# Optimization experiments

Hardware: AMD Instinct MI355X
Metric: run time of the kernel (lower is better)

## Reference

```python
import jax, jax.numpy as jnp
import numpy as np

B, D_IN, H, A, L, HEADS, C = 1024, 512, 768, 5001, 4, 2, 2
N_DATA = 56000.0
NEG = -1e30


def _gru_step(x, h, Wih, Whh, bih, bhh):
    # torch nn.GRU gate order: r, z, n
    gi = x @ Wih + bih            # [B, 3H]
    gh = h @ Whh + bhh            # [B, 3H]
    i_r, i_z, i_n = jnp.split(gi, 3, axis=-1)
    h_r, h_z, h_n = jnp.split(gh, 3, axis=-1)
    r = jax.nn.sigmoid(i_r + h_r)
    z = jax.nn.sigmoid(i_z + h_z)
    n = jnp.tanh(i_n + r * h_n)
    return (1.0 - z) * n + z * h


def _atom_selector(cls, mask, Wih, Whh, bih, bhh, hW, hb, ae_w, key):
    # cls: [B, H]; mask: [B, A] int32 (mutable copy); dropout in eval mode (identity)
    h = jnp.zeros_like(cls)
    cur_in = cls
    ae_const = jax.lax.stop_gradient(ae_w)
    probs = []
    max_index = None
    rows = jnp.arange(B)
    for j in range(L):
        h = _gru_step(cur_in, h, Wih, Whh, bih, bhh)
        logits = h @ hW + hb                      # [B, A]
        if j == 0:
            col0 = jnp.where(mask.sum(axis=-1) == 0, 1, mask[:, 0])
            mask = mask.at[:, 0].set(col0)
        else:
            mask = jnp.where((max_index == 0)[:, None], 0, mask)
            mask = mask.at[:, 0].set(1)
        masked = jnp.where(mask > 0, logits, NEG)
        u = jax.random.uniform(jax.random.fold_in(key, j), (B, A), minval=1e-9, maxval=1.0)
        g = -jnp.log(-jnp.log(u))
        y_soft = jax.nn.softmax(masked + g, axis=-1)  # tau = 1
        ind = jnp.argmax(y_soft, axis=-1)             # [B]
        y_hard = jax.nn.one_hot(ind, A, dtype=y_soft.dtype)
        prob = y_hard + y_soft - jax.lax.stop_gradient(y_soft)  # straight-through
        mask = mask.at[rows, ind].set(0)              # scatter-zero chosen atoms
        probs.append(prob)
        max_index = ind
        cur_in = cls + prob @ ae_const                # atom embedding feedback
    return jnp.stack(probs, axis=1)                   # [B, L, A]


def reference(x, x_mask, W1, b1, W2, b2, W3, b3, gru_Wih, gru_Whh, gru_bih, gru_bhh,
              head_W, head_b, ae_w, ce_Wmu, ce_bmu, ce_Wcov, ce_bcov, alpha):
    # linear_base MLP
    h = jax.nn.relu(x @ W1 + b1)
    h = jax.nn.relu(h @ W2 + b2)
    h = h @ W3 + b3                                   # cls embedding [B, H]
    key = jax.random.key(42)
    atom_probs, cps = [], []
    for i in range(HEADS):
        ap = _atom_selector(h, x_mask, gru_Wih[i], gru_Whh[i], gru_bih[i], gru_bhh[i],
                            head_W[i], head_b[i], ae_w, jax.random.fold_in(key, i))
        atom_probs.append(ap)
        # consequent estimator stand-in: mu [B,C], coverage [B]
        pooled = ap.mean(axis=1)                      # [B, A]
        mu = jax.nn.sigmoid(pooled @ ce_Wmu + ce_bmu)
        coverage = jax.nn.sigmoid(pooled @ ce_Wcov + ce_bcov)
        n = coverage * N_DATA
        sf = (alpha[0] / n)[:, None]                  # [B, 1] -> broadcast to [B, C]
        cp = (mu + sf) / (1.0 + 2.0 * sf)
        cps.append(cp)
    mat_cp = jnp.stack(cps, axis=1)                   # [B, HEADS, C]
    out = jnp.log(mat_cp.mean(axis=1))                # [B, C]
    return out, jnp.stack(atom_probs, axis=1), mat_cp


def setup_inputs() -> dict:
    key = jax.random.key(0)
    ks = jax.random.split(key, 16)
    s = 0.02
    nrm = lambda k, sh: jax.random.normal(k, sh, dtype=jnp.float32) * s
    return {
        'x': jax.random.normal(ks[0], (B, D_IN), dtype=jnp.float32),
        'x_mask': jax.random.randint(ks[1], (B, A), 0, 2, dtype=jnp.int32),
        'W1': nrm(ks[2], (D_IN, H)), 'b1': jnp.zeros((H,), jnp.float32),
        'W2': nrm(ks[3], (H, H)), 'b2': jnp.zeros((H,), jnp.float32),
        'W3': nrm(ks[4], (H, H)), 'b3': jnp.zeros((H,), jnp.float32),
        'gru_Wih': nrm(ks[5], (HEADS, H, 3 * H)), 'gru_Whh': nrm(ks[6], (HEADS, H, 3 * H)),
        'gru_bih': jnp.zeros((HEADS, 3 * H), jnp.float32), 'gru_bhh': jnp.zeros((HEADS, 3 * H), jnp.float32),
        'head_W': nrm(ks[7], (HEADS, H, A)), 'head_b': jnp.zeros((HEADS, A), jnp.float32),
        'ae_w': nrm(ks[8], (A, H)),
        'ce_Wmu': nrm(ks[9], (A, C)), 'ce_bmu': jnp.zeros((C,), jnp.float32),
        'ce_Wcov': nrm(ks[10], (A,)), 'ce_bcov': jnp.zeros((), jnp.float32),
        'alpha': jnp.ones((1,), jnp.float32),
    }
```

## Files before the change

### kernel.cpp

```cpp
#include <hip/hip_runtime.h>
#include <hip/hip_bf16.h>
#include <stdint.h>
#include <stddef.h>

#define B_DIM   1024
#define DIN     512
#define H_DIM   768
#define A_DIM   5001
#define NHEADS  2
#define NSTEPS  4
#define C_DIM   2
#define NEG_VAL -1e30f
#define BH      (B_DIM * H_DIM)

typedef unsigned short u16;
typedef __attribute__((ext_vector_type(8))) short v8s;
typedef __attribute__((ext_vector_type(4))) float v4f;

typedef const __attribute__((address_space(1))) uint32_t* gas_ptr;
typedef __attribute__((address_space(3))) uint32_t* las_ptr;

__device__ __forceinline__ void load_lds16(const void* g, void* l) {
  __builtin_amdgcn_global_load_lds((gas_ptr)g, (las_ptr)l, 16, 0, 0);
}

__host__ __device__ inline uint32_t rotl32(uint32_t x, int d) {
  return (x << d) | (x >> (32 - d));
}

__host__ __device__ inline void threefry2x32(uint32_t k0, uint32_t k1,
                                             uint32_t x0, uint32_t x1,
                                             uint32_t& o0, uint32_t& o1) {
  uint32_t ks2 = k0 ^ k1 ^ 0x1BD11BDAu;
  x0 += k0; x1 += k1;
#define TFR(d) { x0 += x1; x1 = rotl32(x1, (d)); x1 ^= x0; }
  TFR(13) TFR(15) TFR(26) TFR(6)  x0 += k1;  x1 += ks2 + 1u;
  TFR(17) TFR(29) TFR(16) TFR(24) x0 += ks2; x1 += k0 + 2u;
  TFR(13) TFR(15) TFR(26) TFR(6)  x0 += k0;  x1 += k1 + 3u;
  TFR(17) TFR(29) TFR(16) TFR(24) x0 += k1;  x1 += ks2 + 4u;
  TFR(13) TFR(15) TFR(26) TFR(6)  x0 += ks2; x1 += k0 + 5u;
#undef TFR
  o0 = x0; o1 = x1;
}

__device__ inline float gumbel_noise(uint32_t k0, uint32_t k1, uint32_t idx) {
  uint32_t o0, o1;
  threefry2x32(k0, k1, 0u, idx, o0, o1);
  uint32_t bits = o0 ^ o1;
  float f = __uint_as_float(0x3f800000u | (bits >> 9)) - 1.0f;
  float u = fmaxf(1e-9f, f * (1.0f - 1e-9f) + 1e-9f);
  return -logf(-logf(u));
}

__device__ inline float sigmoidf_(float x) { return 0.5f * tanhf(0.5f * x) + 0.5f; }

__device__ inline void split_bf16(float x, u16& hi, u16& lo) {
  __hip_bfloat16 h = __float2bfloat16(x);
  float hf = __bfloat162float(h);
  __hip_bfloat16 l = __float2bfloat16(x - hf);
  hi = *(const u16*)&h;
  lo = *(const u16*)&l;
}

__global__ __launch_bounds__(256) void split_kernel(
    const float* __restrict__ in, u16* __restrict__ hi, u16* __restrict__ lo, int n) {
  int idx = blockIdx.x * blockDim.x + threadIdx.x;
  if (idx >= n) return;
  u16 h, l;
  split_bf16(in[idx], h, l);
  hi[idx] = h; lo[idx] = l;
}

struct TS { const float* W; u16* hi; u16* lo; int K; int N; };
struct TS9 { TS t[9]; };

__global__ __launch_bounds__(256) void transpose_split_b(TS9 ts) {
  const TS p = ts.t[blockIdx.z];
  const int k0 = blockIdx.y * 32, n0 = blockIdx.x * 32;
  if (k0 >= p.K || n0 >= p.N) return;
  __shared__ float tile[32][33];
  const int tx = threadIdx.x & 31, ty = threadIdx.x >> 5;
#pragma unroll
  for (int r = ty; r < 32; r += 8) {
    int n = n0 + tx;
    tile[r][tx] = (n < p.N) ? p.W[(size_t)(k0 + r) * p.N + n] : 0.0f;
  }
  __syncthreads();
#pragma unroll
  for (int r = ty; r < 32; r += 8) {
    int n = n0 + r, k = k0 + tx;
    if (n < p.N) {
      u16 h, l;
      split_bf16(tile[tx][r], h, l);
      p.hi[(size_t)n * p.K + k] = h;
      p.lo[(size_t)n * p.K + k] = l;
    }
  }
}

struct GemmS {
  const u16* Ah[4]; const u16* Al[4];
  const u16* Bh[4]; const u16* Bl[4];
  const float* bias[4];
  float* C[4];
  u16* Ch[4]; u16* Cl[4];
  int N[4]; int nbx[4]; long long ldc[4]; int act[4]; int dup[4];
};

__global__ __launch_bounds__(256, 2) void gemm_mfma(GemmS gs, int K, int nby) {
  const int e = blockIdx.y;
  const int nwg = gridDim.x;
  const int chunk = nwg >> 3;
  const int lid = (blockIdx.x & 7) * chunk + (blockIdx.x >> 3);
  const int by = lid % nby;
  const int bx = lid / nby;
  if (bx >= gs.nbx[e]) return;
  const int bm = by * 128, bn = bx * 128;
  const int N = gs.N[e];

  __shared__ __align__(16) u16 lds[4][128 * 64];

  const int tid = threadIdx.x;
  const int wv = tid >> 6, ln = tid & 63;
  const int wr = wv >> 1, wc = wv & 1;
  const int lk = ln >> 4;
  const int lm = ln & 15;

  const int lrow8 = ln >> 3;
  const int sslot = (ln & 7) ^ lrow8;
  const u16* tsrc = (wv == 0) ? gs.Ah[e] : (wv == 1) ? gs.Al[e]
                  : (wv == 2) ? gs.Bh[e] : gs.Bl[e];
  const int isB = (wv >= 2);
  const int rowbase = isB ? bn : bm;

  v4f acc[4][4];
#pragma unroll
  for (int i = 0; i < 4; ++i)
#pragma unroll
    for (int j = 0; j < 4; ++j) acc[i][j] = (v4f){0.f, 0.f, 0.f, 0.f};

  for (int k0 = 0; k0 < K; k0 += 64) {
#pragma unroll
    for (int i = 0; i < 16; ++i) {
      int gr = rowbase + i * 8 + lrow8;
      if (isB && gr >= N) gr = N - 1;
      const u16* gp = tsrc + (size_t)gr * K + k0 + sslot * 8;
      load_lds16(gp, (void*)&lds[wv][i * 512]);
    }
    __syncthreads();

#pragma unroll
    for (int kh = 0; kh < 2; ++kh) {
      v8s ah[4], al[4], bh[4], bl[4];
#pragma unroll
      for (int mi = 0; mi < 4; ++mi) {
        const int r = wr * 64 + mi * 16 + lm;
        const int off = r * 64 + (((kh * 4 + lk) ^ (r & 7)) * 8);
        ah[mi] = *(const v8s*)&lds[0][off];
        al[mi] = *(const v8s*)&lds[1][off];
      }
#pragma unroll
      for (int ni = 0; ni < 4; ++ni) {
        const int r = wc * 64 + ni * 16 + lm;
        const int off = r * 64 + (((kh * 4 + lk) ^ (r & 7)) * 8);
        bh[ni] = *(const v8s*)&lds[2][off];
        bl[ni] = *(const v8s*)&lds[3][off];
      }
#pragma unroll
      for (int mi = 0; mi < 4; ++mi)
#pragma unroll
        for (int ni = 0; ni < 4; ++ni)
          acc[mi][ni] = __builtin_amdgcn_mfma_f32_16x16x32_bf16(ah[mi], bh[ni], acc[mi][ni], 0, 0, 0);
#pragma unroll
      for (int mi = 0; mi < 4; ++mi)
#pragma unroll
        for (int ni = 0; ni < 4; ++ni)
          acc[mi][ni] = __builtin_amdgcn_mfma_f32_16x16x32_bf16(ah[mi], bl[ni], acc[mi][ni], 0, 0, 0);
#pragma unroll
      for (int mi = 0; mi < 4; ++mi)
#pragma unroll
        for (int ni = 0; ni < 4; ++ni)
          acc[mi][ni] = __builtin_amdgcn_mfma_f32_16x16x32_bf16(al[mi], bh[ni], acc[mi][ni], 0, 0, 0);
    }

    __syncthreads();
  }

  const float* bias = gs.bias[e];
  const long long ldc = gs.ldc[e];
  const int act = gs.act[e];
  float* Cf = gs.C[e];
  u16* ch = gs.Ch[e]; u16* cl = gs.Cl[e];
  const int dup = gs.dup[e];
#pragma unroll
  for (int mi = 0; mi < 4; ++mi) {
    const int m = bm + wr * 64 + mi * 16 + lk * 4;
#pragma unroll
    for (int ni = 0; ni < 4; ++ni) {
      const int n = bn + wc * 64 + ni * 16 + lm;
      if (n < N) {
        const float bv = bias[n];
#pragma unroll
        for (int r = 0; r < 4; ++r) {
          float v = acc[mi][ni][r] + bv;
          if (act) v = fmaxf(v, 0.0f);
          const size_t ix = (size_t)(m + r) * ldc + n;
          if (Cf) Cf[ix] = v;
          if (ch) {
            u16 hh, ll;
            split_bf16(v, hh, ll);
            ch[ix] = hh; cl[ix] = ll;
            if (dup) { ch[ix + (size_t)BH] = hh; cl[ix + (size_t)BH] = ll; }
          }
        }
      }
    }
  }
}

__global__ __launch_bounds__(256) void gru_combine_first(
    const float* __restrict__ gi2, const float* __restrict__ gbhh, float* __restrict__ h2,
    u16* __restrict__ h_hi, u16* __restrict__ h_lo) {
  int idx = blockIdx.x * blockDim.x + threadIdx.x;
  if (idx >= 2 * BH) return;
  int e = idx / BH, rem = idx % BH;
  int b = rem / H_DIM, c = rem - b * H_DIM;
  const float* gib = gi2 + ((size_t)e * B_DIM + b) * 3 * H_DIM;
  const float* bb = gbhh + (size_t)e * 3 * H_DIM;
  float ir = gib[c], iz = gib[H_DIM + c], inn = gib[2 * H_DIM + c];
  float hr = bb[c], hz = bb[H_DIM + c], hn = bb[2 * H_DIM + c];
  float r = sigmoidf_(ir + hr);
  float z = sigmoidf_(iz + hz);
  float n = tanhf(inn + r * hn);
  float hv = (1.0f - z) * n + z * 0.0f;
  h2[idx] = hv;
  u16 h, l;
  split_bf16(hv, h, l);
  h_hi[idx] = h; h_lo[idx] = l;
}

__global__ __launch_bounds__(256) void gru_combine_kernel(
    const float* __restrict__ gi2, const float* __restrict__ gh2, float* __restrict__ h2,
    u16* __restrict__ h_hi, u16* __restrict__ h_lo) {
  int idx = blockIdx.x * blockDim.x + threadIdx.x;
  if (idx >= 2 * BH) return;
  int e = idx / BH, rem = idx % BH;
  int b = rem / H_DIM, c = rem - b * H_DIM;
  const float* gib = gi2 + ((size_t)e * B_DIM + b) * 3 * H_DIM;
  const float* ghb = gh2 + ((size_t)e * B_DIM + b) * 3 * H_DIM;
  float ir = gib[c], iz = gib[H_DIM + c], inn = gib[2 * H_DIM + c];
  float hr = ghb[c], hz = ghb[H_DIM + c], hn = ghb[2 * H_DIM + c];
  float r = sigmoidf_(ir + hr);
  float z = sigmoidf_(iz + hz);
  float n = tanhf(inn + r * hn);
  float hv = (1.0f - z) * n + z * h2[idx];
  h2[idx] = hv;
  u16 h, l;
  split_bf16(hv, h, l);
  h_hi[idx] = h; h_lo[idx] = l;
}

#define STH 256
#define PER_TH 20

__global__ __launch_bounds__(STH) void sample_kernel(
    float* __restrict__ probs, const int* __restrict__ x_mask,
    int* __restrict__ indb, int j, uint4 keys,
    const float* __restrict__ cls, const float* __restrict__ ae_w,
    u16* __restrict__ cur_hi, u16* __restrict__ cur_lo, int docur) {
  int b = blockIdx.x;
  int e = blockIdx.y;
  int t = threadIdx.x;
  uint32_t k0 = (e == 0) ? keys.x : keys.z;
  uint32_t k1 = (e == 0) ? keys.y : keys.w;
  __shared__ float rv[STH];
  __shared__ int ri[STH];
  __shared__ int s_ind;

  float* prow = probs + (((size_t)b * NHEADS + e) * NSTEPS + j) * A_DIM;
  const int* mrow = x_mask + (size_t)b * A_DIM;

  int prev[3];
  bool dead = false;
  for (int tt = 0; tt < j; ++tt) {
    prev[tt] = indb[(e * NSTEPS + tt) * B_DIM + b];
    if (prev[tt] == 0) dead = true;
  }

  bool rowany = true;
  if (j == 0) {
    int any = 0;
    for (int a = t; a < A_DIM; a += STH) any |= mrow[a];
    ri[t] = any; __syncthreads();
    for (int s = STH / 2; s > 0; s >>= 1) {
      if (t < s) ri[t] |= ri[t + s];
      __syncthreads();
    }
    rowany = (ri[0] != 0);
    __syncthreads();
  }

  float v[PER_TH];
  float lmax = -3.0e38f;
#pragma unroll
  for (int s = 0; s < PER_TH; ++s) {
    int a = t + s * STH;
    float val = -3.0e38f;
    if (a < A_DIM) {
      int m;
      if (j == 0) {
        m = (a == 0) ? (rowany ? mrow[0] : 1) : mrow[a];
      } else if (a == 0) {
        m = 1;
      } else if (dead) {
        m = 0;
      } else {
        m = mrow[a];
        if (m) {
          for (int tt = 0; tt < j; ++tt)
            if (prev[tt] == a) { m = 0; break; }
        }
      }
      if (m > 0)
        val = prow[a] + gumbel_noise(k0, k1, (uint32_t)(b * A_DIM + a));
    }
    v[s] = val;
    lmax = fmaxf(lmax, val);
  }

  rv[t] = lmax; __syncthreads();
  for (int s = STH / 2; s > 0; s >>= 1) {
    if (t < s) rv[t] = fmaxf(rv[t], rv[t + s]);
    __syncthreads();
  }
  float m = rv[0]; __syncthreads();

  float lsum = 0.0f;
#pragma unroll
  for (int s = 0; s < PER_TH; ++s) {
    int a = t + s * STH;
    float ev = (a < A_DIM && v[s] > -1.0e37f) ? expf(v[s] - m) : 0.0f;
    v[s] = ev; lsum += ev;
  }
  rv[t] = lsum; __syncthreads();
  for (int s = STH / 2; s > 0; s >>= 1) {
    if (t < s) rv[t] += rv[t + s];
    __syncthreads();
  }
  float ssum = rv[0]; __syncthreads();

  float besty = -1.0f; int besti = A_DIM;
#pragma unroll
  for (int s = 0; s < PER_TH; ++s) {
    int a = t + s * STH;
    if (a < A_DIM) {
      float y = v[s] / ssum;
      if (y > besty) { besty = y; besti = a; }
    }
  }
  rv[t] = besty; ri[t] = besti; __syncthreads();
  for (int s = STH / 2; s > 0; s >>= 1) {
    if (t < s) {
      float y2 = rv[t + s]; int i2 = ri[t + s];
      if (y2 > rv[t] || (y2 == rv[t] && i2 < ri[t])) { rv[t] = y2; ri[t] = i2; }
    }
    __syncthreads();
  }
  if (t == 0) { s_ind = ri[0]; indb[(e * NSTEPS + j) * B_DIM + b] = ri[0]; }
  __syncthreads();
  int ind = s_ind;

  for (int a = t; a < A_DIM; a += STH) prow[a] = (a == ind) ? 1.0f : 0.0f;

  if (docur) {
    const float* crow = cls + (size_t)b * H_DIM;
    const float* arow = ae_w + (size_t)ind * H_DIM;
    u16* chh = cur_hi + (size_t)e * BH + (size_t)b * H_DIM;
    u16* cll = cur_lo + (size_t)e * BH + (size_t)b * H_DIM;
    for (int c = t; c < H_DIM; c += STH) {
      float vv = crow[c] + arow[c];
      u16 hh, ll;
      split_bf16(vv, hh, ll);
      chh[c] = hh; cll[c] = ll;
    }
  }
}

__global__ __launch_bounds__(256) void head_final_kernel(
    const int* __restrict__ indb, const float* __restrict__ Wmu,
    const float* __restrict__ bmu, const float* __restrict__ Wcov,
    const float* __restrict__ bcov, const float* __restrict__ alpha,
    float* __restrict__ matcp) {
  int idx = blockIdx.x * blockDim.x + threadIdx.x;
  if (idx >= NHEADS * B_DIM) return;
  int e = idx / B_DIM, b = idx - e * B_DIM;
  float a0 = 0.0f, a1 = 0.0f, ac = 0.0f;
  for (int j = 0; j < NSTEPS; ++j) {
    int ind = indb[(e * NSTEPS + j) * B_DIM + b];
    a0 += 0.25f * Wmu[(size_t)ind * C_DIM + 0];
    a1 += 0.25f * Wmu[(size_t)ind * C_DIM + 1];
    ac += 0.25f * Wcov[ind];
  }
  float mu0 = sigmoidf_(a0 + bmu[0]);
  float mu1 = sigmoidf_(a1 + bmu[1]);
  float cov = sigmoidf_(ac + bcov[0]);
  float n = cov * 56000.0f;
  float sf = alpha[0] / n;
  float denom = 1.0f + 2.0f * sf;
  matcp[((size_t)b * NHEADS + e) * C_DIM + 0] = (mu0 + sf) / denom;
  matcp[((size_t)b * NHEADS + e) * C_DIM + 1] = (mu1 + sf) / denom;
}

__global__ __launch_bounds__(256) void final_out_kernel(
    const float* __restrict__ matcp, float* __restrict__ out) {
  int idx = blockIdx.x * blockDim.x + threadIdx.x;
  if (idx >= B_DIM * C_DIM) return;
  int b = idx / C_DIM, c = idx - b * C_DIM;
  float s = matcp[((size_t)b * NHEADS + 0) * C_DIM + c] +
            matcp[((size_t)b * NHEADS + 1) * C_DIM + c];
  out[idx] = logf(s * 0.5f);
}

extern "C" void kernel_launch(void* const* d_in, const int* in_sizes, int n_in,
                              void* d_out, int out_size, void* d_ws, size_t ws_size,
                              hipStream_t stream) {
  const float* x     = (const float*)d_in[0];
  const int*   xmask = (const int*)d_in[1];
  const float* W1 = (const float*)d_in[2];  const float* b1 = (const float*)d_in[3];
  const float* W2 = (const float*)d_in[4];  const float* b2 = (const float*)d_in[5];
  const float* W3 = (const float*)d_in[6];  const float* b3 = (const float*)d_in[7];
  const float* gWih = (const float*)d_in[8];  const float* gWhh = (const float*)d_in[9];
  const float* gbih = (const float*)d_in[10]; const float* gbhh = (const float*)d_in[11];
  const float* hW = (const float*)d_in[12];   const float* hb = (const float*)d_in[13];
  const float* ae_w = (const float*)d_in[14];
  const float* Wmu  = (const float*)d_in[15]; const float* bmu  = (const float*)d_in[16];
  const float* Wcov = (const float*)d_in[17]; const float* bcov = (const float*)d_in[18];
  const float* alpha = (const float*)d_in[19];

  float* out = (float*)d_out;
  float* probs = out + (size_t)B_DIM * C_DIM;
  float* matcp = probs + (size_t)B_DIM * NHEADS * NSTEPS * A_DIM;

  const int HG = 3 * H_DIM;
  uint8_t* wsp = (uint8_t*)d_ws;
  auto alloc = [&](size_t bytes) {
    uint8_t* p = wsp;
    wsp += (bytes + 255) & ~(size_t)255;
    return p;
  };
  float* cls  = (float*)alloc((size_t)BH * 4);
  float* h2   = (float*)alloc((size_t)2 * BH * 4);
  float* gi2  = (float*)alloc((size_t)2 * B_DIM * HG * 4);
  float* gh2  = (float*)alloc((size_t)2 * B_DIM * HG * 4);
  u16* h_hi   = (u16*)alloc((size_t)2 * BH * 2);
  u16* h_lo   = (u16*)alloc((size_t)2 * BH * 2);
  u16* cur_hi = (u16*)alloc((size_t)2 * BH * 2);
  u16* cur_lo = (u16*)alloc((size_t)2 * BH * 2);
  u16* WihT_h = (u16*)alloc((size_t)2 * HG * H_DIM * 2);
  u16* WihT_l = (u16*)alloc((size_t)2 * HG * H_DIM * 2);
  u16* WhhT_h = (u16*)alloc((size_t)2 * HG * H_DIM * 2);
  u16* WhhT_l = (u16*)alloc((size_t)2 * HG * H_DIM * 2);
  u16* hWT_h  = (u16*)alloc((size_t)2 * A_DIM * H_DIM * 2);
  u16* hWT_l  = (u16*)alloc((size_t)2 * A_DIM * H_DIM * 2);
  u16* x_hi   = (u16*)alloc((size_t)B_DIM * DIN * 2);
  u16* x_lo   = (u16*)alloc((size_t)B_DIM * DIN * 2);
  u16* t1_hi  = (u16*)alloc((size_t)BH * 2);
  u16* t1_lo  = (u16*)alloc((size_t)BH * 2);
  u16* t2_hi  = (u16*)alloc((size_t)BH * 2);
  u16* t2_lo  = (u16*)alloc((size_t)BH * 2);
  u16* W1T_h  = (u16*)alloc((size_t)H_DIM * DIN * 2);
  u16* W1T_l  = (u16*)alloc((size_t)H_DIM * DIN * 2);
  u16* W2T_h  = (u16*)alloc((size_t)H_DIM * H_DIM * 2);
  u16* W2T_l  = (u16*)alloc((size_t)H_DIM * H_DIM * 2);
  u16* W3T_h  = (u16*)alloc((size_t)H_DIM * H_DIM * 2);
  u16* W3T_l  = (u16*)alloc((size_t)H_DIM * H_DIM * 2);
  int* indb   = (int*)alloc((size_t)NHEADS * NSTEPS * B_DIM * 4);

  dim3 blk(256);

  {
    TS9 ts;
    ts.t[0] = {gWih,                    WihT_h,                    WihT_l,                    H_DIM, HG};
    ts.t[1] = {gWih + (size_t)H_DIM*HG, WihT_h + (size_t)HG*H_DIM, WihT_l + (size_t)HG*H_DIM, H_DIM, HG};
    ts.t[2] = {gWhh,                    WhhT_h,                    WhhT_l,                    H_DIM, HG};
    ts.t[3] = {gWhh + (size_t)H_DIM*HG, WhhT_h + (size_t)HG*H_DIM, WhhT_l + (size_t)HG*H_DIM, H_DIM, HG};
    ts.t[4] = {hW,                          hWT_h,                           hWT_l,                           H_DIM, A_DIM};
    ts.t[5] = {hW + (size_t)H_DIM*A_DIM,    hWT_h + (size_t)A_DIM*H_DIM,     hWT_l + (size_t)A_DIM*H_DIM,     H_DIM, A_DIM};
    ts.t[6] = {W1, W1T_h, W1T_l, DIN,   H_DIM};
    ts.t[7] = {W2, W2T_h, W2T_l, H_DIM, H_DIM};
    ts.t[8] = {W3, W3T_h, W3T_l, H_DIM, H_DIM};
    transpose_split_b<<<dim3((A_DIM + 31) / 32, H_DIM / 32, 9), blk, 0, stream>>>(ts);
  }
  split_kernel<<<(B_DIM * DIN + 255) / 256, blk, 0, stream>>>(x, x_hi, x_lo, B_DIM * DIN);

  auto setE = [](GemmS& g, int e, const u16* ah, const u16* al, const u16* bhp, const u16* blp,
                 const float* bias, float* Cf, u16* chp, u16* clp,
                 int N, int nbx, long long ldc, int act, int dup) {
    g.Ah[e] = ah; g.Al[e] = al; g.Bh[e] = bhp; g.Bl[e] = blp;
    g.bias[e] = bias; g.C[e] = Cf; g.Ch[e] = chp; g.Cl[e] = clp;
    g.N[e] = N; g.nbx[e] = nbx; g.ldc[e] = ldc; g.act[e] = act; g.dup[e] = dup;
  };

  {
    GemmS g{};
    setE(g, 0, x_hi, x_lo, W1T_h, W1T_l, b1, nullptr, t1_hi, t1_lo, H_DIM, H_DIM / 128, H_DIM, 1, 0);
    gemm_mfma<<<dim3((H_DIM / 128) * 8, 1), blk, 0, stream>>>(g, DIN, 8);
  }
  {
    GemmS g{};
    setE(g, 0, t1_hi, t1_lo, W2T_h, W2T_l, b2, nullptr, t2_hi, t2_lo, H_DIM, H_DIM / 128, H_DIM, 1, 0);
    gemm_mfma<<<dim3((H_DIM / 128) * 8, 1), blk, 0, stream>>>(g, H_DIM, 8);
  }
  {
    GemmS g{};
    setE(g, 0, t2_hi, t2_lo, W3T_h, W3T_l, b3, cls, cur_hi, cur_lo, H_DIM, H_DIM / 128, H_DIM, 0, 1);
    gemm_mfma<<<dim3((H_DIM / 128) * 8, 1), blk, 0, stream>>>(g, H_DIM, 8);
  }

  uint32_t bk0 = 0u, bk1 = 42u;
  uint32_t hk[2][2];
  threefry2x32(bk0, bk1, 0u, 0u, hk[0][0], hk[0][1]);
  threefry2x32(bk0, bk1, 0u, 1u, hk[1][0], hk[1][1]);

  const int NBX_L = (A_DIM + 127) / 128;
  const int NBX_G = HG / 128;

  for (int j = 0; j < NSTEPS; ++j) {
    {
      GemmS g{};
      for (int head = 0; head < NHEADS; ++head)
        setE(g, head, cur_hi + (size_t)head * BH, cur_lo + (size_t)head * BH,
             WihT_h + (size_t)head * HG * H_DIM, WihT_l + (size_t)head * HG * H_DIM,
             gbih + (size_t)head * HG, gi2 + (size_t)head * B_DIM * HG, nullptr, nullptr,
             HG, NBX_G, HG, 0, 0);
      gemm_mfma<<<dim3(NBX_G * 8, 2), blk, 0, stream>>>(g, H_DIM, 8);
    }

    if (j == 0)
      gru_combine_first<<<(2 * BH + 255) / 256, blk, 0, stream>>>(gi2, gbhh, h2, h_hi, h_lo);
    else
      gru_combine_kernel<<<(2 * BH + 255) / 256, blk, 0, stream>>>(gi2, gh2, h2, h_hi, h_lo);

    {
      GemmS g{};
      for (int head = 0; head < NHEADS; ++head)
        setE(g, head, h_hi + (size_t)head * BH, h_lo + (size_t)head * BH,
             hWT_h + (size_t)head * A_DIM * H_DIM, hWT_l + (size_t)head * A_DIM * H_DIM,
             hb + (size_t)head * A_DIM, probs + (size_t)(head * NSTEPS + j) * A_DIM,
             nullptr, nullptr, A_DIM, NBX_L, (long long)NHEADS * NSTEPS * A_DIM, 0, 0);
      if (j < NSTEPS - 1) {
        for (int head = 0; head < NHEADS; ++head)
          setE(g, 2 + head, h_hi + (size_t)head * BH, h_lo + (size_t)head * BH,
               WhhT_h + (size_t)head * HG * H_DIM, WhhT_l + (size_t)head * HG * H_DIM,
               gbhh + (size_t)head * HG, gh2 + (size_t)head * B_DIM * HG, nullptr, nullptr,
               HG, NBX_G, HG, 0, 0);
        gemm_mfma<<<dim3(NBX_L * 8, 4), blk, 0, stream>>>(g, H_DIM, 8);
      } else {
        gemm_mfma<<<dim3(NBX_L * 8, 2), blk, 0, stream>>>(g, H_DIM, 8);
      }
    }

    uint32_t s00, s01, s10, s11;
    threefry2x32(hk[0][0], hk[0][1], 0u, (uint32_t)j, s00, s01);
    threefry2x32(hk[1][0], hk[1][1], 0u, (uint32_t)j, s10, s11);
    uint4 keys; keys.x = s00; keys.y = s01; keys.z = s10; keys.w = s11;
    sample_kernel<<<dim3(B_DIM, NHEADS), dim3(STH), 0, stream>>>(
        probs, xmask, indb, j, keys, cls, ae_w, cur_hi, cur_lo, (j < NSTEPS - 1) ? 1 : 0);
  }

  head_final_kernel<<<(NHEADS * B_DIM + 255) / 256, blk, 0, stream>>>(
      indb, Wmu, bmu, Wcov, bcov, alpha, matcp);
  final_out_kernel<<<(B_DIM * C_DIM + 255) / 256, blk, 0, stream>>>(matcp, out);
}
```

Before: 870.8 us.

## Double-buffer GEMM LDS tiles with K=32 stages and regroup GRU hidden GEMM launches

The MFMA GEMM now uses two LDS buffers of 32-wide K slices and prefetches the next slice with async global-to-LDS loads while computing on the current one. This drops the trailing barrier and changes the swizzle to suit the narrower rows. The Whh hidden-state GEMM moves out of the big logits launch and into the next step's input-gate GEMM launch, so the logits grid no longer carries a skewed mix of large and small problems. The cost is more loop iterations with smaller MFMA batches per barrier, and a different launch balance.

```diff
diff --git a/kernel.cpp b/kernel.cpp
--- a/kernel.cpp
+++ b/kernel.cpp
@@ -118,72 +118,81 @@
   const int bm = by * 128, bn = bx * 128;
   const int N = gs.N[e];
 
-  __shared__ __align__(16) u16 lds[4][128 * 64];
+  __shared__ __align__(16) u16 lds[2][4][128 * 32];
 
   const int tid = threadIdx.x;
   const int wv = tid >> 6, ln = tid & 63;
   const int wr = wv >> 1, wc = wv & 1;
   const int lk = ln >> 4;
   const int lm = ln & 15;
-
-  const int lrow8 = ln >> 3;
-  const int sslot = (ln & 7) ^ lrow8;
+  const int fswz = (lm >> 1) & 3;
+
+  const int lrow = ln >> 2;
+  const int slot = (ln & 3) ^ ((lrow >> 1) & 3);
   const u16* tsrc = (wv == 0) ? gs.Ah[e] : (wv == 1) ? gs.Al[e]
                   : (wv == 2) ? gs.Bh[e] : gs.Bl[e];
   const int isB = (wv >= 2);
   const int rowbase = isB ? bn : bm;
 
+#define STAGE(B, K0)                                                  \
+  {                                                                   \
+    _Pragma("unroll")                                                 \
+    for (int i = 0; i < 8; ++i) {                                     \
+      int gr = rowbase + i * 16 + lrow;                               \
+      if (isB && gr >= N) gr = N - 1;                                 \
+      load_lds16(tsrc + (size_t)gr * K + (K0) + slot * 8,             \
+                 (void*)&lds[B][wv][i * 512]);                        \
+    }                                                                 \
+  }
+
   v4f acc[4][4];
 #pragma unroll
   for (int i = 0; i < 4; ++i)
 #pragma unroll
     for (int j = 0; j < 4; ++j) acc[i][j] = (v4f){0.f, 0.f, 0.f, 0.f};
 
-  for (int k0 = 0; k0 < K; k0 += 64) {
-#pragma unroll
-    for (int i = 0; i < 16; ++i) {
-      int gr = rowbase + i * 8 + lrow8;
-      if (isB && gr >= N) gr = N - 1;
-      const u16* gp = tsrc + (size_t)gr * K + k0 + sslot * 8;
-      load_lds16(gp, (void*)&lds[wv][i * 512]);
-    }
+  STAGE(0, 0)
+  int buf = 0;
+  for (int k0 = 0; k0 < K; k0 += 32) {
     __syncthreads();
-
-#pragma unroll
-    for (int kh = 0; kh < 2; ++kh) {
-      v8s ah[4], al[4], bh[4], bl[4];
-#pragma unroll
-      for (int mi = 0; mi < 4; ++mi) {
-        const int r = wr * 64 + mi * 16 + lm;
-        const int off = r * 64 + (((kh * 4 + lk) ^ (r & 7)) * 8);
-        ah[mi] = *(const v8s*)&lds[0][off];
-        al[mi] = *(const v8s*)&lds[1][off];
-      }
-#pragma unroll
-      for (int ni = 0; ni < 4; ++ni) {
-        const int r = wc * 64 + ni * 16 + lm;
-        const int off = r * 64 + (((kh * 4 + lk) ^ (r & 7)) * 8);
-        bh[ni] = *(const v8s*)&lds[2][off];
-        bl[ni] = *(const v8s*)&lds[3][off];
-      }
-#pragma unroll
-      for (int mi = 0; mi < 4; ++mi)
-#pragma unroll
-        for (int ni = 0; ni < 4; ++ni)
-          acc[mi][ni] = __builtin_amdgcn_mfma_f32_16x16x32_bf16(ah[mi], bh[ni], acc[mi][ni], 0, 0, 0);
-#pragma unroll
-      for (int mi = 0; mi < 4; ++mi)
-#pragma unroll
-        for (int ni = 0; ni < 4; ++ni)
-          acc[mi][ni] = __builtin_amdgcn_mfma_f32_16x16x32_bf16(ah[mi], bl[ni], acc[mi][ni], 0, 0, 0);
-#pragma unroll
-      for (int mi = 0; mi < 4; ++mi)
-#pragma unroll
-        for (int ni = 0; ni < 4; ++ni)
-          acc[mi][ni] = __builtin_amdgcn_mfma_f32_16x16x32_bf16(al[mi], bh[ni], acc[mi][ni], 0, 0, 0);
-    }
-
-    __syncthreads();
+    if (k0 + 32 < K) STAGE(buf ^ 1, k0 + 32)
+
+    const u16* LAh = lds[buf][0];
+    const u16* LAl = lds[buf][1];
+    const u16* LBh = lds[buf][2];
+    const u16* LBl = lds[buf][3];
+    v8s ah[4], al[4], bh[4], bl[4];
+#pragma unroll
+    for (int mi = 0; mi < 4; ++mi) {
+      const int r = wr * 64 + mi * 16 + lm;
+      const int off = r * 32 + ((lk ^ fswz) * 8);
+      ah[mi] = *(const v8s*)&LAh[off];
+      al[mi] = *(const v8s*)&LAl[off];
+    }
+#pragma unroll
+    for (int ni = 0; ni < 4; ++ni) {
+      const int r = wc * 64 + ni * 16 + lm;
+      const int off = r * 32 + ((lk ^ fswz) * 8);
+      bh[ni] = *(const v8s*)&LBh[off];
+      bl[ni] = *(const v8s*)&LBl[off];
+    }
+#pragma unroll
+    for (int mi = 0; mi < 4; ++mi)
+#pragma unroll
+      for (int ni = 0; ni < 4; ++ni)
+        acc[mi][ni] = __builtin_amdgcn_mfma_f32_16x16x32_bf16(ah[mi], bh[ni], acc[mi][ni], 0, 0, 0);
+#pragma unroll
+    for (int mi = 0; mi < 4; ++mi)
+#pragma unroll
+      for (int ni = 0; ni < 4; ++ni)
+        acc[mi][ni] = __builtin_amdgcn_mfma_f32_16x16x32_bf16(ah[mi], bl[ni], acc[mi][ni], 0, 0, 0);
+#pragma unroll
+    for (int mi = 0; mi < 4; ++mi)
+#pragma unroll
+      for (int ni = 0; ni < 4; ++ni)
+        acc[mi][ni] = __builtin_amdgcn_mfma_f32_16x16x32_bf16(al[mi], bh[ni], acc[mi][ni], 0, 0, 0);
+
+    buf ^= 1;
   }
 
   const float* bias = gs.bias[e];
@@ -216,6 +225,7 @@
       }
     }
   }
+#undef STAGE
 }
 
 __global__ __launch_bounds__(256) void gru_combine_first(
@@ -526,7 +536,7 @@
   const int NBX_G = HG / 128;
 
   for (int j = 0; j < NSTEPS; ++j) {
-    {
+    if (j == 0) {
       GemmS g{};
       for (int head = 0; head < NHEADS; ++head)
         setE(g, head, cur_hi + (size_t)head * BH, cur_lo + (size_t)head * BH,
@@ -534,12 +544,22 @@
              gbih + (size_t)head * HG, gi2 + (size_t)head * B_DIM * HG, nullptr, nullptr,
              HG, NBX_G, HG, 0, 0);
       gemm_mfma<<<dim3(NBX_G * 8, 2), blk, 0, stream>>>(g, H_DIM, 8);
-    }
-
-    if (j == 0)
       gru_combine_first<<<(2 * BH + 255) / 256, blk, 0, stream>>>(gi2, gbhh, h2, h_hi, h_lo);
-    else
+    } else {
+      GemmS g{};
+      for (int head = 0; head < NHEADS; ++head) {
+        setE(g, head * 2 + 0, cur_hi + (size_t)head * BH, cur_lo + (size_t)head * BH,
+             WihT_h + (size_t)head * HG * H_DIM, WihT_l + (size_t)head * HG * H_DIM,
+             gbih + (size_t)head * HG, gi2 + (size_t)head * B_DIM * HG, nullptr, nullptr,
+             HG, NBX_G, HG, 0, 0);
+        setE(g, head * 2 + 1, h_hi + (size_t)head * BH, h_lo + (size_t)head * BH,
+             WhhT_h + (size_t)head * HG * H_DIM, WhhT_l + (size_t)head * HG * H_DIM,
+             gbhh + (size_t)head * HG, gh2 + (size_t)head * B_DIM * HG, nullptr, nullptr,
+             HG, NBX_G, HG, 0, 0);
+      }
+      gemm_mfma<<<dim3(NBX_G * 8, 4), blk, 0, stream>>>(g, H_DIM, 8);
       gru_combine_kernel<<<(2 * BH + 255) / 256, blk, 0, stream>>>(gi2, gh2, h2, h_hi, h_lo);
+    }
 
     {
       GemmS g{};
@@ -548,16 +568,7 @@
              hWT_h + (size_t)head * A_DIM * H_DIM, hWT_l + (size_t)head * A_DIM * H_DIM,
              hb + (size_t)head * A_DIM, probs + (size_t)(head * NSTEPS + j) * A_DIM,
              nullptr, nullptr, A_DIM, NBX_L, (long long)NHEADS * NSTEPS * A_DIM, 0, 0);
-      if (j < NSTEPS - 1) {
-        for (int head = 0; head < NHEADS; ++head)
-          setE(g, 2 + head, h_hi + (size_t)head * BH, h_lo + (size_t)head * BH,
-               WhhT_h + (size_t)head * HG * H_DIM, WhhT_l + (size_t)head * HG * H_DIM,
-               gbhh + (size_t)head * HG, gh2 + (size_t)head * B_DIM * HG, nullptr, nullptr,
-               HG, NBX_G, HG, 0, 0);
-        gemm_mfma<<<dim3(NBX_L * 8, 4), blk, 0, stream>>>(g, H_DIM, 8);
-      } else {
-        gemm_mfma<<<dim3(NBX_L * 8, 2), blk, 0, stream>>>(g, H_DIM, 8);
-      }
+      gemm_mfma<<<dim3(NBX_L * 8, 2), blk, 0, stream>>>(g, H_DIM, 8);
     }
 
     uint32_t s00, s01, s10, s11;
```

Result: no change. 865.8 us (-0.6%).

## Split GEMM K dimension in two and reduce partial sums in consumers

Applied to the files above, without the earlier changes.

The GEMM gains per-entry K ranges, and each GRU and logits GEMM is split into two K halves that write separate fp32 partial buffers. The GRU combine and sampling kernels add the two partials when they read them. The K tile shrinks from 64 to 32 with a matching LDS swizzle, and the Whh GEMM is regrouped so it launches with the next step's Wih GEMM rather than with the logits GEMM. The aim is more workgroups to fill the CUs on these small-M GEMMs, at the cost of extra partial-sum traffic, a larger workspace and more frequent barriers.

```diff
diff --git a/kernel.cpp b/kernel.cpp
--- a/kernel.cpp
+++ b/kernel.cpp
@@ -12,6 +12,7 @@
 #define C_DIM   2
 #define NEG_VAL -1e30f
 #define BH      (B_DIM * H_DIM)
+#define HG      (3 * H_DIM)
 
 typedef unsigned short u16;
 typedef __attribute__((ext_vector_type(8))) short v8s;
@@ -99,12 +100,13 @@
 }
 
 struct GemmS {
-  const u16* Ah[4]; const u16* Al[4];
-  const u16* Bh[4]; const u16* Bl[4];
-  const float* bias[4];
-  float* C[4];
-  u16* Ch[4]; u16* Cl[4];
-  int N[4]; int nbx[4]; long long ldc[4]; int act[4]; int dup[4];
+  const u16* Ah[8]; const u16* Al[8];
+  const u16* Bh[8]; const u16* Bl[8];
+  const float* bias[8];
+  float* C[8];
+  u16* Ch[8]; u16* Cl[8];
+  int N[8]; int nbx[8]; long long ldc[8]; int act[8]; int dup[8];
+  int k0[8]; int klen[8];
 };
 
 __global__ __launch_bounds__(256, 2) void gemm_mfma(GemmS gs, int K, int nby) {
@@ -117,17 +119,20 @@
   if (bx >= gs.nbx[e]) return;
   const int bm = by * 128, bn = bx * 128;
   const int N = gs.N[e];
-
-  __shared__ __align__(16) u16 lds[4][128 * 64];
+  const int kb = gs.k0[e];
+  const int ke = kb + gs.klen[e];
+
+  __shared__ __align__(16) u16 lds[4][128 * 32];
 
   const int tid = threadIdx.x;
   const int wv = tid >> 6, ln = tid & 63;
   const int wr = wv >> 1, wc = wv & 1;
   const int lk = ln >> 4;
   const int lm = ln & 15;
-
-  const int lrow8 = ln >> 3;
-  const int sslot = (ln & 7) ^ lrow8;
+  const int fswz = (lm >> 1) & 3;
+
+  const int lrow = ln >> 2;
+  const int slot = (ln & 3) ^ ((lrow >> 1) & 3);
   const u16* tsrc = (wv == 0) ? gs.Ah[e] : (wv == 1) ? gs.Al[e]
                   : (wv == 2) ? gs.Bh[e] : gs.Bl[e];
   const int isB = (wv >= 2);
@@ -139,49 +144,46 @@
 #pragma unroll
     for (int j = 0; j < 4; ++j) acc[i][j] = (v4f){0.f, 0.f, 0.f, 0.f};
 
-  for (int k0 = 0; k0 < K; k0 += 64) {
-#pragma unroll
-    for (int i = 0; i < 16; ++i) {
-      int gr = rowbase + i * 8 + lrow8;
+  for (int kt = kb; kt < ke; kt += 32) {
+#pragma unroll
+    for (int i = 0; i < 8; ++i) {
+      int gr = rowbase + i * 16 + lrow;
       if (isB && gr >= N) gr = N - 1;
-      const u16* gp = tsrc + (size_t)gr * K + k0 + sslot * 8;
+      const u16* gp = tsrc + (size_t)gr * K + kt + slot * 8;
       load_lds16(gp, (void*)&lds[wv][i * 512]);
     }
     __syncthreads();
 
-#pragma unroll
-    for (int kh = 0; kh < 2; ++kh) {
-      v8s ah[4], al[4], bh[4], bl[4];
-#pragma unroll
-      for (int mi = 0; mi < 4; ++mi) {
-        const int r = wr * 64 + mi * 16 + lm;
-        const int off = r * 64 + (((kh * 4 + lk) ^ (r & 7)) * 8);
-        ah[mi] = *(const v8s*)&lds[0][off];
-        al[mi] = *(const v8s*)&lds[1][off];
-      }
-#pragma unroll
-      for (int ni = 0; ni < 4; ++ni) {
-        const int r = wc * 64 + ni * 16 + lm;
-        const int off = r * 64 + (((kh * 4 + lk) ^ (r & 7)) * 8);
-        bh[ni] = *(const v8s*)&lds[2][off];
-        bl[ni] = *(const v8s*)&lds[3][off];
-      }
-#pragma unroll
-      for (int mi = 0; mi < 4; ++mi)
-#pragma unroll
-        for (int ni = 0; ni < 4; ++ni)
-          acc[mi][ni] = __builtin_amdgcn_mfma_f32_16x16x32_bf16(ah[mi], bh[ni], acc[mi][ni], 0, 0, 0);
-#pragma unroll
-      for (int mi = 0; mi < 4; ++mi)
-#pragma unroll
-        for (int ni = 0; ni < 4; ++ni)
-          acc[mi][ni] = __builtin_amdgcn_mfma_f32_16x16x32_bf16(ah[mi], bl[ni], acc[mi][ni], 0, 0, 0);
-#pragma unroll
-      for (int mi = 0; mi < 4; ++mi)
-#pragma unroll
-        for (int ni = 0; ni < 4; ++ni)
-          acc[mi][ni] = __builtin_amdgcn_mfma_f32_16x16x32_bf16(al[mi], bh[ni], acc[mi][ni], 0, 0, 0);
-    }
+    v8s ah[4], al[4], bh[4], bl[4];
+#pragma unroll
+    for (int mi = 0; mi < 4; ++mi) {
+      const int r = wr * 64 + mi * 16 + lm;
+      const int off = r * 32 + ((lk ^ fswz) * 8);
+      ah[mi] = *(const v8s*)&lds[0][off];
+      al[mi] = *(const v8s*)&lds[1][off];
+    }
+#pragma unroll
+    for (int ni = 0; ni < 4; ++ni) {
+      const int r = wc * 64 + ni * 16 + lm;
+      const int off = r * 32 + ((lk ^ fswz) * 8);
+      bh[ni] = *(const v8s*)&lds[2][off];
+      bl[ni] = *(const v8s*)&lds[3][off];
+    }
+#pragma unroll
+    for (int mi = 0; mi < 4; ++mi)
+#pragma unroll
+      for (int ni = 0; ni < 4; ++ni)
+        acc[mi][ni] = __builtin_amdgcn_mfma_f32_16x16x32_bf16(ah[mi], bh[ni], acc[mi][ni], 0, 0, 0);
+#pragma unroll
+    for (int mi = 0; mi < 4; ++mi)
+#pragma unroll
+      for (int ni = 0; ni < 4; ++ni)
+        acc[mi][ni] = __builtin_amdgcn_mfma_f32_16x16x32_bf16(ah[mi], bl[ni], acc[mi][ni], 0, 0, 0);
+#pragma unroll
+    for (int mi = 0; mi < 4; ++mi)
+#pragma unroll
+      for (int ni = 0; ni < 4; ++ni)
+        acc[mi][ni] = __builtin_amdgcn_mfma_f32_16x16x32_bf16(al[mi], bh[ni], acc[mi][ni], 0, 0, 0);
 
     __syncthreads();
   }
@@ -199,7 +201,7 @@
     for (int ni = 0; ni < 4; ++ni) {
       const int n = bn + wc * 64 + ni * 16 + lm;
       if (n < N) {
-        const float bv = bias[n];
+        const float bv = bias ? bias[n] : 0.0f;
 #pragma unroll
         for (int r = 0; r < 4; ++r) {
           float v = acc[mi][ni][r] + bv;
@@ -219,15 +221,18 @@
 }
 
 __global__ __launch_bounds__(256) void gru_combine_first(
-    const float* __restrict__ gi2, const float* __restrict__ gbhh, float* __restrict__ h2,
+    const float* __restrict__ gip, const float* __restrict__ gbhh, float* __restrict__ h2,
     u16* __restrict__ h_hi, u16* __restrict__ h_lo) {
   int idx = blockIdx.x * blockDim.x + threadIdx.x;
   if (idx >= 2 * BH) return;
   int e = idx / BH, rem = idx % BH;
   int b = rem / H_DIM, c = rem - b * H_DIM;
-  const float* gib = gi2 + ((size_t)e * B_DIM + b) * 3 * H_DIM;
-  const float* bb = gbhh + (size_t)e * 3 * H_DIM;
-  float ir = gib[c], iz = gib[H_DIM + c], inn = gib[2 * H_DIM + c];
+  const float* g0 = gip + ((size_t)(0 * 2 + e) * B_DIM + b) * HG;
+  const float* g1 = gip + ((size_t)(1 * 2 + e) * B_DIM + b) * HG;
+  const float* bb = gbhh + (size_t)e * HG;
+  float ir = g0[c] + g1[c];
+  float iz = g0[H_DIM + c] + g1[H_DIM + c];
+  float inn = g0[2 * H_DIM + c] + g1[2 * H_DIM + c];
   float hr = bb[c], hz = bb[H_DIM + c], hn = bb[2 * H_DIM + c];
   float r = sigmoidf_(ir + hr);
   float z = sigmoidf_(iz + hz);
@@ -240,16 +245,22 @@
 }
 
 __global__ __launch_bounds__(256) void gru_combine_kernel(
-    const float* __restrict__ gi2, const float* __restrict__ gh2, float* __restrict__ h2,
+    const float* __restrict__ gip, const float* __restrict__ ghp, float* __restrict__ h2,
     u16* __restrict__ h_hi, u16* __restrict__ h_lo) {
   int idx = blockIdx.x * blockDim.x + threadIdx.x;
   if (idx >= 2 * BH) return;
   int e = idx / BH, rem = idx % BH;
   int b = rem / H_DIM, c = rem - b * H_DIM;
-  const float* gib = gi2 + ((size_t)e * B_DIM + b) * 3 * H_DIM;
-  const float* ghb = gh2 + ((size_t)e * B_DIM + b) * 3 * H_DIM;
-  float ir = gib[c], iz = gib[H_DIM + c], inn = gib[2 * H_DIM + c];
-  float hr = ghb[c], hz = ghb[H_DIM + c], hn = ghb[2 * H_DIM + c];
+  const float* gi0 = gip + ((size_t)(0 * 2 + e) * B_DIM + b) * HG;
+  const float* gi1 = gip + ((size_t)(1 * 2 + e) * B_DIM + b) * HG;
+  const float* gh0 = ghp + ((size_t)(0 * 2 + e) * B_DIM + b) * HG;
+  const float* gh1 = ghp + ((size_t)(1 * 2 + e) * B_DIM + b) * HG;
+  float ir = gi0[c] + gi1[c];
+  float iz = gi0[H_DIM + c] + gi1[H_DIM + c];
+  float inn = gi0[2 * H_DIM + c] + gi1[2 * H_DIM + c];
+  float hr = gh0[c] + gh1[c];
+  float hz = gh0[H_DIM + c] + gh1[H_DIM + c];
+  float hn = gh0[2 * H_DIM + c] + gh1[2 * H_DIM + c];
   float r = sigmoidf_(ir + hr);
   float z = sigmoidf_(iz + hz);
   float n = tanhf(inn + r * hn);
@@ -264,7 +275,7 @@
 #define PER_TH 20
 
 __global__ __launch_bounds__(STH) void sample_kernel(
-    float* __restrict__ probs, const int* __restrict__ x_mask,
+    const float* __restrict__ lp, float* __restrict__ probs, const int* __restrict__ x_mask,
     int* __restrict__ indb, int j, uint4 keys,
     const float* __restrict__ cls, const float* __restrict__ ae_w,
     u16* __restrict__ cur_hi, u16* __restrict__ cur_lo, int docur) {
@@ -277,6 +288,8 @@
   __shared__ int ri[STH];
   __shared__ int s_ind;
 
+  const float* l0 = lp + ((size_t)(0 * 2 + e) * B_DIM + b) * A_DIM;
+  const float* l1 = lp + ((size_t)(1 * 2 + e) * B_DIM + b) * A_DIM;
   float* prow = probs + (((size_t)b * NHEADS + e) * NSTEPS + j) * A_DIM;
   const int* mrow = x_mask + (size_t)b * A_DIM;
 
@@ -322,7 +335,7 @@
         }
       }
       if (m > 0)
-        val = prow[a] + gumbel_noise(k0, k1, (uint32_t)(b * A_DIM + a));
+        val = l0[a] + l1[a] + gumbel_noise(k0, k1, (uint32_t)(b * A_DIM + a));
     }
     v[s] = val;
     lmax = fmaxf(lmax, val);
@@ -441,7 +454,6 @@
   float* probs = out + (size_t)B_DIM * C_DIM;
   float* matcp = probs + (size_t)B_DIM * NHEADS * NSTEPS * A_DIM;
 
-  const int HG = 3 * H_DIM;
   uint8_t* wsp = (uint8_t*)d_ws;
   auto alloc = [&](size_t bytes) {
     uint8_t* p = wsp;
@@ -450,8 +462,9 @@
   };
   float* cls  = (float*)alloc((size_t)BH * 4);
   float* h2   = (float*)alloc((size_t)2 * BH * 4);
-  float* gi2  = (float*)alloc((size_t)2 * B_DIM * HG * 4);
-  float* gh2  = (float*)alloc((size_t)2 * B_DIM * HG * 4);
+  float* gi2  = (float*)alloc((size_t)4 * B_DIM * HG * 4);
+  float* gh2  = (float*)alloc((size_t)4 * B_DIM * HG * 4);
+  float* lp   = (float*)alloc((size_t)4 * B_DIM * A_DIM * 4);
   u16* h_hi   = (u16*)alloc((size_t)2 * BH * 2);
   u16* h_lo   = (u16*)alloc((size_t)2 * BH * 2);
   u16* cur_hi = (u16*)alloc((size_t)2 * BH * 2);
@@ -495,25 +508,26 @@
 
   auto setE = [](GemmS& g, int e, const u16* ah, const u16* al, const u16* bhp, const u16* blp,
                  const float* bias, float* Cf, u16* chp, u16* clp,
-                 int N, int nbx, long long ldc, int act, int dup) {
+                 int N, int nbx, long long ldc, int act, int dup, int k0, int klen) {
     g.Ah[e] = ah; g.Al[e] = al; g.Bh[e] = bhp; g.Bl[e] = blp;
     g.bias[e] = bias; g.C[e] = Cf; g.Ch[e] = chp; g.Cl[e] = clp;
     g.N[e] = N; g.nbx[e] = nbx; g.ldc[e] = ldc; g.act[e] = act; g.dup[e] = dup;
+    g.k0[e] = k0; g.klen[e] = klen;
   };
 
   {
     GemmS g{};
-    setE(g, 0, x_hi, x_lo, W1T_h, W1T_l, b1, nullptr, t1_hi, t1_lo, H_DIM, H_DIM / 128, H_DIM, 1, 0);
+    setE(g, 0, x_hi, x_lo, W1T_h, W1T_l, b1, nullptr, t1_hi, t1_lo, H_DIM, H_DIM / 128, H_DIM, 1, 0, 0, DIN);
     gemm_mfma<<<dim3((H_DIM / 128) * 8, 1), blk, 0, stream>>>(g, DIN, 8);
   }
   {
     GemmS g{};
-    setE(g, 0, t1_hi, t1_lo, W2T_h, W2T_l, b2, nullptr, t2_hi, t2_lo, H_DIM, H_DIM / 128, H_DIM, 1, 0);
+    setE(g, 0, t1_hi, t1_lo, W2T_h, W2T_l, b2, nullptr, t2_hi, t2_lo, H_DIM, H_DIM / 128, H_DIM, 1, 0, 0, H_DIM);
     gemm_mfma<<<dim3((H_DIM / 128) * 8, 1), blk, 0, stream>>>(g, H_DIM, 8);
   }
   {
     GemmS g{};
-    setE(g, 0, t2_hi, t2_lo, W3T_h, W3T_l, b3, cls, cur_hi, cur_lo, H_DIM, H_DIM / 128, H_DIM, 0, 1);
+    setE(g, 0, t2_hi, t2_lo, W3T_h, W3T_l, b3, cls, cur_hi, cur_lo, H_DIM, H_DIM / 128, H_DIM, 0, 1, 0, H_DIM);
     gemm_mfma<<<dim3((H_DIM / 128) * 8, 1), blk, 0, stream>>>(g, H_DIM, 8);
   }
 
@@ -524,40 +538,49 @@
 
   const int NBX_L = (A_DIM + 127) / 128;
   const int NBX_G = HG / 128;
+  const int KH = H_DIM / 2;
 
   for (int j = 0; j < NSTEPS; ++j) {
+    if (j == 0) {
+      GemmS g{};
+      for (int head = 0; head < NHEADS; ++head)
+        for (int c = 0; c < 2; ++c)
+          setE(g, head * 2 + c, cur_hi + (size_t)head * BH, cur_lo + (size_t)head * BH,
+               WihT_h + (size_t)head * HG * H_DIM, WihT_l + (size_t)head * HG * H_DIM,
+               c == 0 ? gbih + (size_t)head * HG : nullptr,
+               gi2 + (size_t)(c * 2 + head) * B_DIM * HG, nullptr, nullptr,
+               HG, NBX_G, HG, 0, 0, c * KH, KH);
+      gemm_mfma<<<dim3(NBX_G * 8, 4), blk, 0, stream>>>(g, H_DIM, 8);
+      gru_combine_first<<<(2 * BH + 255) / 256, blk, 0, stream>>>(gi2, gbhh, h2, h_hi, h_lo);
+    } else {
+      GemmS g{};
+      for (int head = 0; head < NHEADS; ++head)
+        for (int src = 0; src < 2; ++src)
+          for (int c = 0; c < 2; ++c) {
+            const u16* ah = src ? h_hi + (size_t)head * BH : cur_hi + (size_t)head * BH;
+            const u16* al = src ? h_lo + (size_t)head * BH : cur_lo + (size_t)head * BH;
+            const u16* bhp = (src ? WhhT_h : WihT_h) + (size_t)head * HG * H_DIM;
+            const u16* blp = (src ? WhhT_l : WihT_l) + (size_t)head * HG * H_DIM;
+            const float* bias = c ? nullptr
+                                  : (src ? gbhh : gbih) + (size_t)head * HG;
+            float* Cf = (src ? gh2 : gi2) + (size_t)(c * 2 + head) * B_DIM * HG;
+            setE(g, ((head * 2 + src) << 1) | c, ah, al, bhp, blp, bias, Cf,
+                 nullptr, nullptr, HG, NBX_G, HG, 0, 0, c * KH, KH);
+          }
+      gemm_mfma<<<dim3(NBX_G * 8, 8), blk, 0, stream>>>(g, H_DIM, 8);
+      gru_combine_kernel<<<(2 * BH + 255) / 256, blk, 0, stream>>>(gi2, gh2, h2, h_hi, h_lo);
+    }
+
     {
       GemmS g{};
       for (int head = 0; head < NHEADS; ++head)
-        setE(g, head, cur_hi + (size_t)head * BH, cur_lo + (size_t)head * BH,
-             WihT_h + (size_t)head * HG * H_DIM, WihT_l + (size_t)head * HG * H_DIM,
-             gbih + (size_t)head * HG, gi2 + (size_t)head * B_DIM * HG, nullptr, nullptr,
-             HG, NBX_G, HG, 0, 0);
-      gemm_mfma<<<dim3(NBX_G * 8, 2), blk, 0, stream>>>(g, H_DIM, 8);
-    }
-
-    if (j == 0)
-      gru_combine_first<<<(2 * BH + 255) / 256, blk, 0, stream>>>(gi2, gbhh, h2, h_hi, h_lo);
-    else
-      gru_combine_kernel<<<(2 * BH + 255) / 256, blk, 0, stream>>>(gi2, gh2, h2, h_hi, h_lo);
-
-    {
-      GemmS g{};
-      for (int head = 0; head < NHEADS; ++head)
-        setE(g, head, h_hi + (size_t)head * BH, h_lo + (size_t)head * BH,
-             hWT_h + (size_t)head * A_DIM * H_DIM, hWT_l + (size_t)head * A_DIM * H_DIM,
-             hb + (size_t)head * A_DIM, probs + (size_t)(head * NSTEPS + j) * A_DIM,
-             nullptr, nullptr, A_DIM, NBX_L, (long long)NHEADS * NSTEPS * A_DIM, 0, 0);
-      if (j < NSTEPS - 1) {
-        for (int head = 0; head < NHEADS; ++head)
-          setE(g, 2 + head, h_hi + (size_t)head * BH, h_lo + (size_t)head * BH,
-               WhhT_h + (size_t)head * HG * H_DIM, WhhT_l + (size_t)head * HG * H_DIM,
-               gbhh + (size_t)head * HG, gh2 + (size_t)head * B_DIM * HG, nullptr, nullptr,
-               HG, NBX_G, HG, 0, 0);
-        gemm_mfma<<<dim3(NBX_L * 8, 4), blk, 0, stream>>>(g, H_DIM, 8);
-      } else {
-        gemm_mfma<<<dim3(NBX_L * 8, 2), blk, 0, stream>>>(g, H_DIM, 8);
-      }
+        for (int c = 0; c < 2; ++c)
+          setE(g, head * 2 + c, h_hi + (size_t)head * BH, h_lo + (size_t)head * BH,
+               hWT_h + (size_t)head * A_DIM * H_DIM, hWT_l + (size_t)head * A_DIM * H_DIM,
+               c == 0 ? hb + (size_t)head * A_DIM : nullptr,
+               lp + (size_t)(c * 2 + head) * B_DIM * A_DIM, nullptr, nullptr,
+               A_DIM, NBX_L, A_DIM, 0, 0, c * KH, KH);
+      gemm_mfma<<<dim3(NBX_L * 8, 4), blk, 0, stream>>>(g, H_DIM, 8);
     }
 
     uint32_t s00, s01, s10, s11;
@@ -565,7 +588,7 @@
     threefry2x32(hk[1][0], hk[1][1], 0u, (uint32_t)j, s10, s11);
     uint4 keys; keys.x = s00; keys.y = s01; keys.z = s10; keys.w = s11;
     sample_kernel<<<dim3(B_DIM, NHEADS), dim3(STH), 0, stream>>>(
-        probs, xmask, indb, j, keys, cls, ae_w, cur_hi, cur_lo, (j < NSTEPS - 1) ? 1 : 0);
+        lp, probs, xmask, indb, j, keys, cls, ae_w, cur_hi, cur_lo, (j < NSTEPS - 1) ? 1 : 0);
   }
 
   head_final_kernel<<<(NHEADS * B_DIM + 255) / 256, blk, 0, stream>>>(
```

New measurement: 940.6 us. 1.08x slower.
